# Kernel tuning notes

Measured on AMD Instinct MI355X. Metric: run time of the kernel, lower is better.

The kernel has to match this reference:

```python
import jax, jax.numpy as jnp
import numpy as np

IN_DIM = 784
HIDDEN = 512
STYLE = 128
BATCH = 2048
NUM_LABELS = 10


def setup_inputs() -> dict:
    key = jax.random.key(0)
    k1, k2, k3, k4 = jax.random.split(key, 4)
    x = jax.random.uniform(k1, (BATCH, IN_DIM), dtype=jnp.float32)
    m = jax.random.randint(k2, (BATCH,), 0, NUM_LABELS)
    # Embedding tables, scaled as in the torch __init__ (N(0,1)/fan)
    fc1_table = jax.random.normal(k3, (NUM_LABELS, (IN_DIM + 1) * HIDDEN), dtype=jnp.float32) / ((IN_DIM + 1) * HIDDEN)
    fc2_table = jax.random.normal(k4, (NUM_LABELS, (HIDDEN + 1) * STYLE), dtype=jnp.float32) / ((HIDDEN + 1) * STYLE)
    return {"x": x, "m": m, "fc1_table": fc1_table, "fc2_table": fc2_table}


def reference(x, m, fc1_table, fc2_table):
    B = x.shape[0]
    x = x.reshape(B, -1)  # [B, 784]
    # Per-sample weight matrices gathered by label
    fc1 = fc1_table[m].reshape(B, IN_DIM + 1, HIDDEN)   # [B, 785, H]
    fc1_w, fc1_b = fc1[:, :IN_DIM, :], fc1[:, -1, :]
    h1 = jax.nn.relu(jnp.einsum('bkj,bk->bj', fc1_w, x) + fc1_b)  # [B, H]
    fc2 = fc2_table[m].reshape(B, HIDDEN + 1, STYLE)    # [B, H+1, S]
    fc2_w, fc2_b = fc2[:, :HIDDEN, :], fc2[:, -1, :]
    h2 = jnp.einsum('bkj,bk->bj', fc2_w, h1) + fc2_b    # [B, S]
    return jax.nn.sigmoid(h2)
```

## Files before the change

### kernel.cpp

```cpp
#include <hip/hip_runtime.h>
#include <hip/hip_bf16.h>
#include <math.h>

#define BATCH      2048
#define IN_DIM     784
#define HIDDEN     512
#define STYLE      128
#define NUM_LABELS 10
#define FC1_STRIDE ((IN_DIM + 1) * HIDDEN)
#define FC2_STRIDE ((HIDDEN + 1) * STYLE)
#define KP1        832

#define TB        64
#define MAX_TILES 48
#define BK        64

#define META_NTILES 31
#define META_TILES  32
#define META_PERM   176

#define W1B_OFF  16384ULL
#define W2B_OFF  (W1B_OFF + 10ULL*HIDDEN*KP1*2)
#define H1B_OFF  (W2B_OFF + 10ULL*STYLE*HIDDEN*2)
#define BF16_NEED (H1B_OFF + (size_t)BATCH*HIDDEN*2)

#define W1_KB 26
#define W1_NB 16
#define W2_KB 16
#define W2_NB 4
#define W1_BLOCKS (W1_KB*W1_NB*NUM_LABELS)
#define W2_BLOCKS (W2_KB*W2_NB*NUM_LABELS)

typedef short short8  __attribute__((ext_vector_type(8)));
typedef float float4e __attribute__((ext_vector_type(4)));

__device__ __forceinline__ ushort f2b(float v) {
    __hip_bfloat16 h = __float2bfloat16(v);
    return *reinterpret_cast<ushort*>(&h);
}

__global__ void k_prep(const int* __restrict__ m, const float* __restrict__ fc1t,
                       const float* __restrict__ fc2t, int* __restrict__ meta,
                       ushort* __restrict__ w1b, ushort* __restrict__ w2b) {
    const int tid = threadIdx.x;
    int bid = blockIdx.x;

    __shared__ int cnt[NUM_LABELS], curs[NUM_LABELS], offs[NUM_LABELS + 1];
    __shared__ int permS[BATCH];
    __shared__ float tile[32][33];

    if (bid == 0) {
        if (tid < NUM_LABELS) { cnt[tid] = 0; curs[tid] = 0; }
        __syncthreads();
        for (int b = tid; b < BATCH; b += 256) atomicAdd(&cnt[m[b]], 1);
        __syncthreads();
        if (tid == 0) {
            int off = 0;
            for (int L = 0; L < NUM_LABELS; ++L) { offs[L] = off; off += cnt[L]; }
            offs[NUM_LABELS] = off;
        }
        __syncthreads();
        for (int b = tid; b < BATCH; b += 256) {
            int L = m[b];
            int r = atomicAdd(&curs[L], 1);
            permS[offs[L] + r] = b;
        }
        __syncthreads();
        for (int i = tid; i < BATCH; i += 256) meta[META_PERM + i] = permS[i];
        if (tid == 0) {
            int idx = 0;
            for (int L = 0; L < NUM_LABELS; ++L) {
                int c = cnt[L], off = offs[L];
                for (int t = 0; t < c; t += TB) {
                    meta[META_TILES + idx * 3 + 0] = L;
                    meta[META_TILES + idx * 3 + 1] = off + t;
                    meta[META_TILES + idx * 3 + 2] = min(TB, c - t);
                    ++idx;
                }
            }
            meta[META_NTILES] = idx;
        }
        return;
    }

    bid -= 1;
    const float* src; ushort* dst; int Kvalid, Kpad, N, kb, nb, L; size_t srcL, dstL;
    if (bid < W1_BLOCKS) {
        kb = bid % W1_KB; nb = (bid / W1_KB) % W1_NB; L = bid / (W1_KB * W1_NB);
        src = fc1t; dst = w1b; Kvalid = IN_DIM; Kpad = KP1; N = HIDDEN;
        srcL = FC1_STRIDE; dstL = (size_t)HIDDEN * KP1;
    } else {
        bid -= W1_BLOCKS;
        kb = bid % W2_KB; nb = (bid / W2_KB) % W2_NB; L = bid / (W2_KB * W2_NB);
        src = fc2t; dst = w2b; Kvalid = HIDDEN; Kpad = HIDDEN; N = STYLE;
        srcL = FC2_STRIDE; dstL = (size_t)STYLE * HIDDEN;
    }
    const int tx = tid & 31, ty = tid >> 5;
    const int k0 = kb * 32, n0 = nb * 32;
    for (int r = ty; r < 32; r += 8) {
        int k = k0 + r;
        tile[r][tx] = (k < Kvalid) ? src[(size_t)L * srcL + (size_t)k * N + n0 + tx] : 0.f;
    }
    __syncthreads();
    for (int r = ty; r < 32; r += 8) {
        int n = n0 + r;
        dst[(size_t)L * dstL + (size_t)n * Kpad + k0 + tx] = f2b(tile[tx][r]);
    }
}

__launch_bounds__(256)
__global__ void k_fc1m(const float* __restrict__ x, const ushort* __restrict__ w1b,
                       const float* __restrict__ fc1t, const int* __restrict__ meta,
                       ushort* __restrict__ h1b) {
    const int t = blockIdx.x;
    if (t >= meta[META_NTILES]) return;
    const int L      = meta[META_TILES + 3 * t + 0];
    const int pstart = meta[META_TILES + 3 * t + 1];
    const int nrows  = meta[META_TILES + 3 * t + 2];
    const int col0   = blockIdx.y * 64;
    const ushort* __restrict__ W = w1b + (size_t)L * HIDDEN * KP1 + (size_t)col0 * KP1;

    __shared__ int rows[TB];
    __shared__ __align__(16) ushort As[64][72];
    __shared__ __align__(16) ushort Bs[64][72];

    const int tid = threadIdx.x;
    if (tid < TB) rows[tid] = (tid < nrows) ? meta[META_PERM + pstart + tid] : -1;
    __syncthreads();

    const int sr = tid >> 2, sc = tid & 3;
    const int lane = tid & 63, wv = tid >> 6;
    const int qd = lane >> 4, ln16 = lane & 15;

    const int arow = rows[sr];
    const float* __restrict__ xr = x + (size_t)(arow < 0 ? 0 : arow) * IN_DIM;
    const uint4* __restrict__ bgp = (const uint4*)(W + (size_t)sr * KP1);

    float4e acc[4] = {};

    for (int k0 = 0; k0 < KP1; k0 += BK) {
        const int ka = k0 + sc * 16;
        float4 a0 = make_float4(0.f, 0.f, 0.f, 0.f), a1 = a0, a2 = a0, a3 = a0;
        if (arow >= 0) {
            if (ka      < IN_DIM) a0 = *(const float4*)(xr + ka);
            if (ka + 4  < IN_DIM) a1 = *(const float4*)(xr + ka + 4);
            if (ka + 8  < IN_DIM) a2 = *(const float4*)(xr + ka + 8);
            if (ka + 12 < IN_DIM) a3 = *(const float4*)(xr + ka + 12);
        }
        uint4 b0 = bgp[(k0 >> 3) + sc * 2 + 0];
        uint4 b1 = bgp[(k0 >> 3) + sc * 2 + 1];

        ushort av[16];
        av[0]=f2b(a0.x); av[1]=f2b(a0.y); av[2]=f2b(a0.z); av[3]=f2b(a0.w);
        av[4]=f2b(a1.x); av[5]=f2b(a1.y); av[6]=f2b(a1.z); av[7]=f2b(a1.w);
        av[8]=f2b(a2.x); av[9]=f2b(a2.y); av[10]=f2b(a2.z); av[11]=f2b(a2.w);
        av[12]=f2b(a3.x); av[13]=f2b(a3.y); av[14]=f2b(a3.z); av[15]=f2b(a3.w);
        *(uint4*)&As[sr][sc * 16 + 0] = *(const uint4*)&av[0];
        *(uint4*)&As[sr][sc * 16 + 8] = *(const uint4*)&av[8];
        *(uint4*)&Bs[sr][sc * 16 + 0] = b0;
        *(uint4*)&Bs[sr][sc * 16 + 8] = b1;
        __syncthreads();
#pragma unroll
        for (int s = 0; s < 2; ++s) {
            short8 a = *(const short8*)&As[wv * 16 + ln16][s * 32 + qd * 8];
#pragma unroll
            for (int nt = 0; nt < 4; ++nt) {
                short8 b = *(const short8*)&Bs[nt * 16 + ln16][s * 32 + qd * 8];
                acc[nt] = __builtin_amdgcn_mfma_f32_16x16x32_bf16(a, b, acc[nt], 0, 0, 0);
            }
        }
        __syncthreads();
    }

    const float* __restrict__ bias = fc1t + (size_t)L * FC1_STRIDE + (size_t)IN_DIM * HIDDEN + col0;
#pragma unroll
    for (int nt = 0; nt < 4; ++nt) {
        const int c = nt * 16 + ln16;
        const float bs = bias[c];
#pragma unroll
        for (int i = 0; i < 4; ++i) {
            const int r = wv * 16 + qd * 4 + i;
            if (r < nrows)
                h1b[(size_t)(pstart + r) * HIDDEN + col0 + c] = f2b(fmaxf(acc[nt][i] + bs, 0.f));
        }
    }
}

__launch_bounds__(256)
__global__ void k_fc2m(const ushort* __restrict__ h1b, const ushort* __restrict__ w2b,
                       const float* __restrict__ fc2t, const int* __restrict__ meta,
                       float* __restrict__ out) {
    const int t = blockIdx.x;
    if (t >= meta[META_NTILES]) return;
    const int L      = meta[META_TILES + 3 * t + 0];
    const int pstart = meta[META_TILES + 3 * t + 1];
    const int nrows  = meta[META_TILES + 3 * t + 2];
    const int col0   = blockIdx.y * 64;
    const ushort* __restrict__ W = w2b + (size_t)L * STYLE * HIDDEN + (size_t)col0 * HIDDEN;

    __shared__ int rows[TB];
    __shared__ __align__(16) ushort As[64][72];
    __shared__ __align__(16) ushort Bs[64][72];

    const int tid = threadIdx.x;
    if (tid < TB) rows[tid] = (tid < nrows) ? meta[META_PERM + pstart + tid] : -1;
    __syncthreads();

    const int sr = tid >> 2, sc = tid & 3;
    const int lane = tid & 63, wv = tid >> 6;
    const int qd = lane >> 4, ln16 = lane & 15;

    const bool aval = (sr < nrows);
    const uint4* __restrict__ agp = (const uint4*)(h1b + (size_t)(pstart + (aval ? sr : 0)) * HIDDEN);
    const uint4* __restrict__ bgp = (const uint4*)(W + (size_t)sr * HIDDEN);

    float4e acc[4] = {};

    for (int k0 = 0; k0 < HIDDEN; k0 += BK) {
        uint4 a0 = make_uint4(0u, 0u, 0u, 0u), a1 = a0;
        if (aval) {
            a0 = agp[(k0 >> 3) + sc * 2 + 0];
            a1 = agp[(k0 >> 3) + sc * 2 + 1];
        }
        uint4 b0 = bgp[(k0 >> 3) + sc * 2 + 0];
        uint4 b1 = bgp[(k0 >> 3) + sc * 2 + 1];
        *(uint4*)&As[sr][sc * 16 + 0] = a0;
        *(uint4*)&As[sr][sc * 16 + 8] = a1;
        *(uint4*)&Bs[sr][sc * 16 + 0] = b0;
        *(uint4*)&Bs[sr][sc * 16 + 8] = b1;
        __syncthreads();
#pragma unroll
        for (int s = 0; s < 2; ++s) {
            short8 a = *(const short8*)&As[wv * 16 + ln16][s * 32 + qd * 8];
#pragma unroll
            for (int nt = 0; nt < 4; ++nt) {
                short8 b = *(const short8*)&Bs[nt * 16 + ln16][s * 32 + qd * 8];
                acc[nt] = __builtin_amdgcn_mfma_f32_16x16x32_bf16(a, b, acc[nt], 0, 0, 0);
            }
        }
        __syncthreads();
    }

    const float* __restrict__ bias = fc2t + (size_t)L * FC2_STRIDE + (size_t)HIDDEN * STYLE + col0;
#pragma unroll
    for (int nt = 0; nt < 4; ++nt) {
        const int c = nt * 16 + ln16;
        const float bs = bias[c];
#pragma unroll
        for (int i = 0; i < 4; ++i) {
            const int r = wv * 16 + qd * 4 + i;
            if (r < nrows) {
                const int orow = rows[r];
                out[(size_t)orow * STYLE + col0 + c] = 1.f / (1.f + __expf(-(acc[nt][i] + bs)));
            }
        }
    }
}

__launch_bounds__(256)
__global__ void k_naive(const float* __restrict__ x, const int* __restrict__ m,
                        const float* __restrict__ fc1t, const float* __restrict__ fc2t,
                        float* __restrict__ out) {
    __shared__ float xs[IN_DIM];
    __shared__ float h1[HIDDEN];
    const int b = blockIdx.x, tid = threadIdx.x, L = m[b];
    for (int k = tid; k < IN_DIM; k += 256) xs[k] = x[(size_t)b * IN_DIM + k];
    __syncthreads();
    const float* __restrict__ W1 = fc1t + (size_t)L * FC1_STRIDE;
    for (int j = tid; j < HIDDEN; j += 256) {
        float acc = W1[(size_t)IN_DIM * HIDDEN + j];
        for (int k = 0; k < IN_DIM; ++k) acc = fmaf(xs[k], W1[(size_t)k * HIDDEN + j], acc);
        h1[j] = fmaxf(acc, 0.f);
    }
    __syncthreads();
    const float* __restrict__ W2 = fc2t + (size_t)L * FC2_STRIDE;
    for (int j = tid; j < STYLE; j += 256) {
        float acc = W2[(size_t)HIDDEN * STYLE + j];
        for (int k = 0; k < HIDDEN; ++k) acc = fmaf(h1[k], W2[(size_t)k * STYLE + j], acc);
        out[(size_t)b * STYLE + j] = 1.f / (1.f + __expf(-acc));
    }
}

extern "C" void kernel_launch(void* const* d_in, const int* in_sizes, int n_in,
                              void* d_out, int out_size, void* d_ws, size_t ws_size,
                              hipStream_t stream) {
    const float* x    = (const float*)d_in[0];
    const int*   m    = (const int*)d_in[1];
    const float* fc1t = (const float*)d_in[2];
    const float* fc2t = (const float*)d_in[3];
    float* out = (float*)d_out;

    if (ws_size >= BF16_NEED) {
        int*    meta = (int*)d_ws;
        ushort* w1b  = (ushort*)((char*)d_ws + W1B_OFF);
        ushort* w2b  = (ushort*)((char*)d_ws + W2B_OFF);
        ushort* h1b  = (ushort*)((char*)d_ws + H1B_OFF);

        k_prep<<<1 + W1_BLOCKS + W2_BLOCKS, 256, 0, stream>>>(m, fc1t, fc2t, meta, w1b, w2b);
        k_fc1m<<<dim3(MAX_TILES, HIDDEN / 64), 256, 0, stream>>>(x, w1b, fc1t, meta, h1b);
        k_fc2m<<<dim3(MAX_TILES, STYLE / 64), 256, 0, stream>>>(h1b, w2b, fc2t, meta, out);
    } else {
        k_naive<<<BATCH, 256, 0, stream>>>(x, m, fc1t, fc2t, out);
    }
}
```

Measured before the change: 107.0 us.

## Fuse prep, fc1 and fc2 into one persistent kernel with grid barriers

Replaces the three launches with one persistent kernel of 512 blocks that does label sorting, x and weight conversion to bf16, the fc1 GEMM and the fc2 GEMM, separated by software grid-wide barriers. x is now pre-converted to padded bf16 once, not converted inside the GEMM loop, and the GEMM loops prefetch the next K-slice into registers while the current one is computed. This removes launch gaps and repeated x conversion. In exchange it relies on all 512 blocks being co-resident for the spin barrier. It also adds the barrier cost and an extra bf16 x buffer in the workspace.

```diff
diff --git a/kernel.cpp b/kernel.cpp
--- a/kernel.cpp
+++ b/kernel.cpp
@@ -10,248 +10,269 @@
 #define FC1_STRIDE ((IN_DIM + 1) * HIDDEN)
 #define FC2_STRIDE ((HIDDEN + 1) * STYLE)
 #define KP1        832
-
-#define TB        64
-#define MAX_TILES 48
-#define BK        64
+#define TB         64
+#define BK         64
+#define NBLK       512
 
 #define META_NTILES 31
 #define META_TILES  32
 #define META_PERM   176
 
-#define W1B_OFF  16384ULL
+#define XB_OFF   16384ULL
+#define W1B_OFF  (XB_OFF  + (size_t)BATCH*KP1*2)
 #define W2B_OFF  (W1B_OFF + 10ULL*HIDDEN*KP1*2)
 #define H1B_OFF  (W2B_OFF + 10ULL*STYLE*HIDDEN*2)
-#define BF16_NEED (H1B_OFF + (size_t)BATCH*HIDDEN*2)
+#define WS_NEED  (H1B_OFF + (size_t)BATCH*HIDDEN*2)
 
 #define W1_KB 26
 #define W1_NB 16
 #define W2_KB 16
 #define W2_NB 4
-#define W1_BLOCKS (W1_KB*W1_NB*NUM_LABELS)
-#define W2_BLOCKS (W2_KB*W2_NB*NUM_LABELS)
+#define W1_TILES (W1_KB*W1_NB*NUM_LABELS)
+#define W2_TILES (W2_KB*W2_NB*NUM_LABELS)
+#define NT_TOT   (W1_TILES + W2_TILES)
+#define XCHUNKS  (BATCH * (KP1/8))
 
 typedef short short8  __attribute__((ext_vector_type(8)));
 typedef float float4e __attribute__((ext_vector_type(4)));
+
+__device__ int g_bar[2];
 
 __device__ __forceinline__ ushort f2b(float v) {
     __hip_bfloat16 h = __float2bfloat16(v);
     return *reinterpret_cast<ushort*>(&h);
 }
 
-__global__ void k_prep(const int* __restrict__ m, const float* __restrict__ fc1t,
-                       const float* __restrict__ fc2t, int* __restrict__ meta,
-                       ushort* __restrict__ w1b, ushort* __restrict__ w2b) {
-    const int tid = threadIdx.x;
-    int bid = blockIdx.x;
-
-    __shared__ int cnt[NUM_LABELS], curs[NUM_LABELS], offs[NUM_LABELS + 1];
-    __shared__ int permS[BATCH];
-    __shared__ float tile[32][33];
-
-    if (bid == 0) {
-        if (tid < NUM_LABELS) { cnt[tid] = 0; curs[tid] = 0; }
-        __syncthreads();
-        for (int b = tid; b < BATCH; b += 256) atomicAdd(&cnt[m[b]], 1);
+__device__ __forceinline__ void grid_sync(int slot) {
+    __threadfence();
+    __syncthreads();
+    if (threadIdx.x == 0) {
+        int ticket = __hip_atomic_fetch_add(&g_bar[slot], 1, __ATOMIC_ACQ_REL,
+                                            __HIP_MEMORY_SCOPE_AGENT);
+        int target = (ticket / NBLK + 1) * NBLK;
+        while (__hip_atomic_load(&g_bar[slot], __ATOMIC_ACQUIRE,
+                                 __HIP_MEMORY_SCOPE_AGENT) < target)
+            __builtin_amdgcn_s_sleep(2);
+    }
+    __syncthreads();
+    __threadfence();
+}
+
+__global__ __launch_bounds__(256, 2)
+void k_fused(const float* __restrict__ x, const int* __restrict__ m,
+             const float* __restrict__ fc1t, const float* __restrict__ fc2t,
+             char* __restrict__ ws, float* __restrict__ out) {
+    int*    meta = (int*)ws;
+    ushort* xb   = (ushort*)(ws + XB_OFF);
+    ushort* w1b  = (ushort*)(ws + W1B_OFF);
+    ushort* w2b  = (ushort*)(ws + W2B_OFF);
+    ushort* h1b  = (ushort*)(ws + H1B_OFF);
+
+    __shared__ __align__(16) char smem[64*72*2*2 + 256];
+    ushort (*As)[72] = (ushort(*)[72])smem;
+    ushort (*Bs)[72] = (ushort(*)[72])(smem + 64*72*2);
+    int*   rowsS     = (int*)(smem + 64*72*2*2);
+    float (*tileS)[36] = (float(*)[36])smem;
+    int* permS = (int*)smem;
+    int* cntS  = (int*)(smem + 8192);
+    int* cursS = (int*)(smem + 8192 + 64);
+    int* offsS = (int*)(smem + 8192 + 128);
+
+    const int tid = threadIdx.x, bid = blockIdx.x;
+
+    if (bid == NBLK - 1) {
+        if (tid < NUM_LABELS) { cntS[tid] = 0; cursS[tid] = 0; }
+        __syncthreads();
+        for (int b = tid; b < BATCH; b += 256) atomicAdd(&cntS[m[b]], 1);
         __syncthreads();
         if (tid == 0) {
             int off = 0;
-            for (int L = 0; L < NUM_LABELS; ++L) { offs[L] = off; off += cnt[L]; }
-            offs[NUM_LABELS] = off;
+            for (int L = 0; L < NUM_LABELS; ++L) { offsS[L] = off; off += cntS[L]; }
+            offsS[NUM_LABELS] = off;
         }
         __syncthreads();
         for (int b = tid; b < BATCH; b += 256) {
             int L = m[b];
-            int r = atomicAdd(&curs[L], 1);
-            permS[offs[L] + r] = b;
+            int r = atomicAdd(&cursS[L], 1);
+            permS[offsS[L] + r] = b;
         }
         __syncthreads();
         for (int i = tid; i < BATCH; i += 256) meta[META_PERM + i] = permS[i];
         if (tid == 0) {
             int idx = 0;
             for (int L = 0; L < NUM_LABELS; ++L) {
-                int c = cnt[L], off = offs[L];
+                int c = cntS[L], off = offsS[L];
                 for (int t = 0; t < c; t += TB) {
-                    meta[META_TILES + idx * 3 + 0] = L;
-                    meta[META_TILES + idx * 3 + 1] = off + t;
-                    meta[META_TILES + idx * 3 + 2] = min(TB, c - t);
+                    meta[META_TILES + idx*3 + 0] = L;
+                    meta[META_TILES + idx*3 + 1] = off + t;
+                    meta[META_TILES + idx*3 + 2] = min(TB, c - t);
                     ++idx;
                 }
             }
             meta[META_NTILES] = idx;
         }
-        return;
-    }
-
-    bid -= 1;
-    const float* src; ushort* dst; int Kvalid, Kpad, N, kb, nb, L; size_t srcL, dstL;
-    if (bid < W1_BLOCKS) {
-        kb = bid % W1_KB; nb = (bid / W1_KB) % W1_NB; L = bid / (W1_KB * W1_NB);
-        src = fc1t; dst = w1b; Kvalid = IN_DIM; Kpad = KP1; N = HIDDEN;
-        srcL = FC1_STRIDE; dstL = (size_t)HIDDEN * KP1;
     } else {
-        bid -= W1_BLOCKS;
-        kb = bid % W2_KB; nb = (bid / W2_KB) % W2_NB; L = bid / (W2_KB * W2_NB);
-        src = fc2t; dst = w2b; Kvalid = HIDDEN; Kpad = HIDDEN; N = STYLE;
-        srcL = FC2_STRIDE; dstL = (size_t)STYLE * HIDDEN;
-    }
-    const int tx = tid & 31, ty = tid >> 5;
-    const int k0 = kb * 32, n0 = nb * 32;
-    for (int r = ty; r < 32; r += 8) {
-        int k = k0 + r;
-        tile[r][tx] = (k < Kvalid) ? src[(size_t)L * srcL + (size_t)k * N + n0 + tx] : 0.f;
-    }
-    __syncthreads();
-    for (int r = ty; r < 32; r += 8) {
-        int n = n0 + r;
-        dst[(size_t)L * dstL + (size_t)n * Kpad + k0 + tx] = f2b(tile[tx][r]);
-    }
-}
-
-__launch_bounds__(256)
-__global__ void k_fc1m(const float* __restrict__ x, const ushort* __restrict__ w1b,
-                       const float* __restrict__ fc1t, const int* __restrict__ meta,
-                       ushort* __restrict__ h1b) {
-    const int t = blockIdx.x;
-    if (t >= meta[META_NTILES]) return;
-    const int L      = meta[META_TILES + 3 * t + 0];
-    const int pstart = meta[META_TILES + 3 * t + 1];
-    const int nrows  = meta[META_TILES + 3 * t + 2];
-    const int col0   = blockIdx.y * 64;
-    const ushort* __restrict__ W = w1b + (size_t)L * HIDDEN * KP1 + (size_t)col0 * KP1;
-
-    __shared__ int rows[TB];
-    __shared__ __align__(16) ushort As[64][72];
-    __shared__ __align__(16) ushort Bs[64][72];
-
-    const int tid = threadIdx.x;
-    if (tid < TB) rows[tid] = (tid < nrows) ? meta[META_PERM + pstart + tid] : -1;
-    __syncthreads();
-
+        for (int u = bid*256 + tid; u < XCHUNKS; u += (NBLK-1)*256) {
+            int row = u / 104, ka = (u - row*104) * 8;
+            uint4 o;
+            if (ka < IN_DIM) {
+                float4 p0 = *(const float4*)(x + (size_t)row*IN_DIM + ka);
+                float4 p1 = *(const float4*)(x + (size_t)row*IN_DIM + ka + 4);
+                ushort t8[8] = {f2b(p0.x), f2b(p0.y), f2b(p0.z), f2b(p0.w),
+                                f2b(p1.x), f2b(p1.y), f2b(p1.z), f2b(p1.w)};
+                o = *(const uint4*)t8;
+            } else o = make_uint4(0u, 0u, 0u, 0u);
+            *(uint4*)(xb + (size_t)row*KP1 + ka) = o;
+        }
+        for (int tt = bid; tt < NT_TOT; tt += NBLK - 1) {
+            const float* src; ushort* dst; int Kv, Kp, N, kb, nb, L; size_t sL, dL;
+            if (tt < W1_TILES) {
+                kb = tt % W1_KB; nb = (tt / W1_KB) % W1_NB; L = tt / (W1_KB * W1_NB);
+                src = fc1t; dst = w1b; Kv = IN_DIM; Kp = KP1; N = HIDDEN;
+                sL = FC1_STRIDE; dL = (size_t)HIDDEN * KP1;
+            } else {
+                int q = tt - W1_TILES;
+                kb = q % W2_KB; nb = (q / W2_KB) % W2_NB; L = q / (W2_KB * W2_NB);
+                src = fc2t; dst = w2b; Kv = HIDDEN; Kp = HIDDEN; N = STYLE;
+                sL = FC2_STRIDE; dL = (size_t)STYLE * HIDDEN;
+            }
+            const int k0 = kb*32, n0 = nb*32;
+            const int row = tid >> 3, c4 = tid & 7;
+            const int gk = k0 + row;
+            float4 v = make_float4(0.f, 0.f, 0.f, 0.f);
+            if (gk < Kv) v = *(const float4*)(src + (size_t)L*sL + (size_t)gk*N + n0 + c4*4);
+            __syncthreads();
+            *(float4*)&tileS[row][c4*4] = v;
+            __syncthreads();
+            const int on = tid >> 3, oc = tid & 7;
+            ushort4 o4;
+            o4.x = f2b(tileS[oc*4+0][on]); o4.y = f2b(tileS[oc*4+1][on]);
+            o4.z = f2b(tileS[oc*4+2][on]); o4.w = f2b(tileS[oc*4+3][on]);
+            *(ushort4*)(dst + (size_t)L*dL + (size_t)(n0+on)*Kp + k0 + oc*4) = o4;
+        }
+    }
+    grid_sync(0);
+
+    const int ntiles = meta[META_NTILES];
     const int sr = tid >> 2, sc = tid & 3;
-    const int lane = tid & 63, wv = tid >> 6;
-    const int qd = lane >> 4, ln16 = lane & 15;
-
-    const int arow = rows[sr];
-    const float* __restrict__ xr = x + (size_t)(arow < 0 ? 0 : arow) * IN_DIM;
-    const uint4* __restrict__ bgp = (const uint4*)(W + (size_t)sr * KP1);
-
-    float4e acc[4] = {};
-
-    for (int k0 = 0; k0 < KP1; k0 += BK) {
-        const int ka = k0 + sc * 16;
-        float4 a0 = make_float4(0.f, 0.f, 0.f, 0.f), a1 = a0, a2 = a0, a3 = a0;
-        if (arow >= 0) {
-            if (ka      < IN_DIM) a0 = *(const float4*)(xr + ka);
-            if (ka + 4  < IN_DIM) a1 = *(const float4*)(xr + ka + 4);
-            if (ka + 8  < IN_DIM) a2 = *(const float4*)(xr + ka + 8);
-            if (ka + 12 < IN_DIM) a3 = *(const float4*)(xr + ka + 12);
-        }
-        uint4 b0 = bgp[(k0 >> 3) + sc * 2 + 0];
-        uint4 b1 = bgp[(k0 >> 3) + sc * 2 + 1];
-
-        ushort av[16];
-        av[0]=f2b(a0.x); av[1]=f2b(a0.y); av[2]=f2b(a0.z); av[3]=f2b(a0.w);
-        av[4]=f2b(a1.x); av[5]=f2b(a1.y); av[6]=f2b(a1.z); av[7]=f2b(a1.w);
-        av[8]=f2b(a2.x); av[9]=f2b(a2.y); av[10]=f2b(a2.z); av[11]=f2b(a2.w);
-        av[12]=f2b(a3.x); av[13]=f2b(a3.y); av[14]=f2b(a3.z); av[15]=f2b(a3.w);
-        *(uint4*)&As[sr][sc * 16 + 0] = *(const uint4*)&av[0];
-        *(uint4*)&As[sr][sc * 16 + 8] = *(const uint4*)&av[8];
-        *(uint4*)&Bs[sr][sc * 16 + 0] = b0;
-        *(uint4*)&Bs[sr][sc * 16 + 8] = b1;
-        __syncthreads();
-#pragma unroll
-        for (int s = 0; s < 2; ++s) {
-            short8 a = *(const short8*)&As[wv * 16 + ln16][s * 32 + qd * 8];
-#pragma unroll
-            for (int nt = 0; nt < 4; ++nt) {
-                short8 b = *(const short8*)&Bs[nt * 16 + ln16][s * 32 + qd * 8];
-                acc[nt] = __builtin_amdgcn_mfma_f32_16x16x32_bf16(a, b, acc[nt], 0, 0, 0);
-            }
-        }
-        __syncthreads();
-    }
-
-    const float* __restrict__ bias = fc1t + (size_t)L * FC1_STRIDE + (size_t)IN_DIM * HIDDEN + col0;
-#pragma unroll
-    for (int nt = 0; nt < 4; ++nt) {
-        const int c = nt * 16 + ln16;
-        const float bs = bias[c];
-#pragma unroll
-        for (int i = 0; i < 4; ++i) {
-            const int r = wv * 16 + qd * 4 + i;
-            if (r < nrows)
-                h1b[(size_t)(pstart + r) * HIDDEN + col0 + c] = f2b(fmaxf(acc[nt][i] + bs, 0.f));
-        }
-    }
-}
-
-__launch_bounds__(256)
-__global__ void k_fc2m(const ushort* __restrict__ h1b, const ushort* __restrict__ w2b,
-                       const float* __restrict__ fc2t, const int* __restrict__ meta,
-                       float* __restrict__ out) {
-    const int t = blockIdx.x;
-    if (t >= meta[META_NTILES]) return;
-    const int L      = meta[META_TILES + 3 * t + 0];
-    const int pstart = meta[META_TILES + 3 * t + 1];
-    const int nrows  = meta[META_TILES + 3 * t + 2];
-    const int col0   = blockIdx.y * 64;
-    const ushort* __restrict__ W = w2b + (size_t)L * STYLE * HIDDEN + (size_t)col0 * HIDDEN;
-
-    __shared__ int rows[TB];
-    __shared__ __align__(16) ushort As[64][72];
-    __shared__ __align__(16) ushort Bs[64][72];
-
-    const int tid = threadIdx.x;
-    if (tid < TB) rows[tid] = (tid < nrows) ? meta[META_PERM + pstart + tid] : -1;
-    __syncthreads();
-
-    const int sr = tid >> 2, sc = tid & 3;
-    const int lane = tid & 63, wv = tid >> 6;
-    const int qd = lane >> 4, ln16 = lane & 15;
-
-    const bool aval = (sr < nrows);
-    const uint4* __restrict__ agp = (const uint4*)(h1b + (size_t)(pstart + (aval ? sr : 0)) * HIDDEN);
-    const uint4* __restrict__ bgp = (const uint4*)(W + (size_t)sr * HIDDEN);
-
-    float4e acc[4] = {};
-
-    for (int k0 = 0; k0 < HIDDEN; k0 += BK) {
-        uint4 a0 = make_uint4(0u, 0u, 0u, 0u), a1 = a0;
-        if (aval) {
-            a0 = agp[(k0 >> 3) + sc * 2 + 0];
-            a1 = agp[(k0 >> 3) + sc * 2 + 1];
-        }
-        uint4 b0 = bgp[(k0 >> 3) + sc * 2 + 0];
-        uint4 b1 = bgp[(k0 >> 3) + sc * 2 + 1];
-        *(uint4*)&As[sr][sc * 16 + 0] = a0;
-        *(uint4*)&As[sr][sc * 16 + 8] = a1;
-        *(uint4*)&Bs[sr][sc * 16 + 0] = b0;
-        *(uint4*)&Bs[sr][sc * 16 + 8] = b1;
-        __syncthreads();
-#pragma unroll
-        for (int s = 0; s < 2; ++s) {
-            short8 a = *(const short8*)&As[wv * 16 + ln16][s * 32 + qd * 8];
-#pragma unroll
-            for (int nt = 0; nt < 4; ++nt) {
-                short8 b = *(const short8*)&Bs[nt * 16 + ln16][s * 32 + qd * 8];
-                acc[nt] = __builtin_amdgcn_mfma_f32_16x16x32_bf16(a, b, acc[nt], 0, 0, 0);
-            }
-        }
-        __syncthreads();
-    }
-
-    const float* __restrict__ bias = fc2t + (size_t)L * FC2_STRIDE + (size_t)HIDDEN * STYLE + col0;
-#pragma unroll
-    for (int nt = 0; nt < 4; ++nt) {
-        const int c = nt * 16 + ln16;
-        const float bs = bias[c];
-#pragma unroll
-        for (int i = 0; i < 4; ++i) {
-            const int r = wv * 16 + qd * 4 + i;
-            if (r < nrows) {
-                const int orow = rows[r];
-                out[(size_t)orow * STYLE + col0 + c] = 1.f / (1.f + __expf(-(acc[nt][i] + bs)));
+    const int lane = tid & 63, wv = tid >> 6, qd = lane >> 4, ln16 = lane & 15;
+
+    for (int j = bid; j < ntiles * 8; j += NBLK) {
+        const int t = j >> 3, cb = j & 7;
+        const int L      = meta[META_TILES + 3*t + 0];
+        const int pstart = meta[META_TILES + 3*t + 1];
+        const int nrows  = meta[META_TILES + 3*t + 2];
+        const int col0   = cb * 64;
+        __syncthreads();
+        if (tid < TB) rowsS[tid] = (tid < nrows) ? meta[META_PERM + pstart + tid] : -1;
+        __syncthreads();
+        const int arow = rowsS[sr];
+        const bool aval = (arow >= 0);
+        const uint4* __restrict__ agp = (const uint4*)(xb + (size_t)(aval ? arow : 0) * KP1);
+        const uint4* __restrict__ bgp = (const uint4*)(w1b + (size_t)L*HIDDEN*KP1 + (size_t)(col0 + sr)*KP1);
+
+        float4e acc[4] = {};
+        uint4 a0, a1, b0, b1;
+        {
+            const int base = sc * 2;
+            a0 = aval ? agp[base] : make_uint4(0u,0u,0u,0u);
+            a1 = aval ? agp[base+1] : make_uint4(0u,0u,0u,0u);
+            b0 = bgp[base]; b1 = bgp[base+1];
+        }
+        for (int it = 0; it < KP1/BK; ++it) {
+            *(uint4*)&As[sr][sc*16 + 0] = a0;
+            *(uint4*)&As[sr][sc*16 + 8] = a1;
+            *(uint4*)&Bs[sr][sc*16 + 0] = b0;
+            *(uint4*)&Bs[sr][sc*16 + 8] = b1;
+            __syncthreads();
+            if (it + 1 < KP1/BK) {
+                const int base = (it+1)*8 + sc*2;
+                a0 = aval ? agp[base] : make_uint4(0u,0u,0u,0u);
+                a1 = aval ? agp[base+1] : make_uint4(0u,0u,0u,0u);
+                b0 = bgp[base]; b1 = bgp[base+1];
+            }
+#pragma unroll
+            for (int s = 0; s < 2; ++s) {
+                short8 af = *(const short8*)&As[wv*16 + ln16][s*32 + qd*8];
+#pragma unroll
+                for (int nt = 0; nt < 4; ++nt) {
+                    short8 bf = *(const short8*)&Bs[nt*16 + ln16][s*32 + qd*8];
+                    acc[nt] = __builtin_amdgcn_mfma_f32_16x16x32_bf16(af, bf, acc[nt], 0, 0, 0);
+                }
+            }
+            __syncthreads();
+        }
+        const float* __restrict__ bias = fc1t + (size_t)L*FC1_STRIDE + (size_t)IN_DIM*HIDDEN + col0;
+#pragma unroll
+        for (int nt = 0; nt < 4; ++nt) {
+            const int c = nt*16 + ln16;
+            const float bs = bias[c];
+#pragma unroll
+            for (int i = 0; i < 4; ++i) {
+                const int r = wv*16 + qd*4 + i;
+                if (r < nrows)
+                    h1b[(size_t)(pstart + r)*HIDDEN + col0 + c] = f2b(fmaxf(acc[nt][i] + bs, 0.f));
+            }
+        }
+    }
+    grid_sync(1);
+
+    for (int j = bid; j < ntiles * 2; j += NBLK) {
+        const int t = j >> 1, cb = j & 1;
+        const int L      = meta[META_TILES + 3*t + 0];
+        const int pstart = meta[META_TILES + 3*t + 1];
+        const int nrows  = meta[META_TILES + 3*t + 2];
+        const int col0   = cb * 64;
+        __syncthreads();
+        if (tid < TB) rowsS[tid] = (tid < nrows) ? meta[META_PERM + pstart + tid] : -1;
+        __syncthreads();
+        const bool aval = (sr < nrows);
+        const uint4* __restrict__ agp = (const uint4*)(h1b + (size_t)(pstart + (aval ? sr : 0))*HIDDEN);
+        const uint4* __restrict__ bgp = (const uint4*)(w2b + (size_t)L*STYLE*HIDDEN + (size_t)(col0 + sr)*HIDDEN);
+
+        float4e acc[4] = {};
+        uint4 a0, a1, b0, b1;
+        {
+            const int base = sc * 2;
+            a0 = aval ? agp[base] : make_uint4(0u,0u,0u,0u);
+            a1 = aval ? agp[base+1] : make_uint4(0u,0u,0u,0u);
+            b0 = bgp[base]; b1 = bgp[base+1];
+        }
+        for (int it = 0; it < HIDDEN/BK; ++it) {
+            *(uint4*)&As[sr][sc*16 + 0] = a0;
+            *(uint4*)&As[sr][sc*16 + 8] = a1;
+            *(uint4*)&Bs[sr][sc*16 + 0] = b0;
+            *(uint4*)&Bs[sr][sc*16 + 8] = b1;
+            __syncthreads();
+            if (it + 1 < HIDDEN/BK) {
+                const int base = (it+1)*8 + sc*2;
+                a0 = aval ? agp[base] : make_uint4(0u,0u,0u,0u);
+                a1 = aval ? agp[base+1] : make_uint4(0u,0u,0u,0u);
+                b0 = bgp[base]; b1 = bgp[base+1];
+            }
+#pragma unroll
+            for (int s = 0; s < 2; ++s) {
+                short8 af = *(const short8*)&As[wv*16 + ln16][s*32 + qd*8];
+#pragma unroll
+                for (int nt = 0; nt < 4; ++nt) {
+                    short8 bf = *(const short8*)&Bs[nt*16 + ln16][s*32 + qd*8];
+                    acc[nt] = __builtin_amdgcn_mfma_f32_16x16x32_bf16(af, bf, acc[nt], 0, 0, 0);
+                }
+            }
+            __syncthreads();
+        }
+        const float* __restrict__ bias = fc2t + (size_t)L*FC2_STRIDE + (size_t)HIDDEN*STYLE + col0;
+#pragma unroll
+        for (int nt = 0; nt < 4; ++nt) {
+            const int c = nt*16 + ln16;
+            const float bs = bias[c];
+#pragma unroll
+            for (int i = 0; i < 4; ++i) {
+                const int r = wv*16 + qd*4 + i;
+                if (r < nrows) {
+                    const int orow = rowsS[r];
+                    out[(size_t)orow*STYLE + col0 + c] = 1.f / (1.f + __expf(-(acc[nt][i] + bs)));
+                }
             }
         }
     }
@@ -264,20 +285,20 @@
     __shared__ float xs[IN_DIM];
     __shared__ float h1[HIDDEN];
     const int b = blockIdx.x, tid = threadIdx.x, L = m[b];
-    for (int k = tid; k < IN_DIM; k += 256) xs[k] = x[(size_t)b * IN_DIM + k];
+    for (int k = tid; k < IN_DIM; k += 256) xs[k] = x[(size_t)b*IN_DIM + k];
     __syncthreads();
-    const float* __restrict__ W1 = fc1t + (size_t)L * FC1_STRIDE;
+    const float* __restrict__ W1 = fc1t + (size_t)L*FC1_STRIDE;
     for (int j = tid; j < HIDDEN; j += 256) {
-        float acc = W1[(size_t)IN_DIM * HIDDEN + j];
-        for (int k = 0; k < IN_DIM; ++k) acc = fmaf(xs[k], W1[(size_t)k * HIDDEN + j], acc);
+        float acc = W1[(size_t)IN_DIM*HIDDEN + j];
+        for (int k = 0; k < IN_DIM; ++k) acc = fmaf(xs[k], W1[(size_t)k*HIDDEN + j], acc);
         h1[j] = fmaxf(acc, 0.f);
     }
     __syncthreads();
-    const float* __restrict__ W2 = fc2t + (size_t)L * FC2_STRIDE;
+    const float* __restrict__ W2 = fc2t + (size_t)L*FC2_STRIDE;
     for (int j = tid; j < STYLE; j += 256) {
-        float acc = W2[(size_t)HIDDEN * STYLE + j];
-        for (int k = 0; k < HIDDEN; ++k) acc = fmaf(h1[k], W2[(size_t)k * STYLE + j], acc);
-        out[(size_t)b * STYLE + j] = 1.f / (1.f + __expf(-acc));
+        float acc = W2[(size_t)HIDDEN*STYLE + j];
+        for (int k = 0; k < HIDDEN; ++k) acc = fmaf(h1[k], W2[(size_t)k*STYLE + j], acc);
+        out[(size_t)b*STYLE + j] = 1.f / (1.f + __expf(-acc));
     }
 }
 
@@ -290,15 +311,8 @@
     const float* fc2t = (const float*)d_in[3];
     float* out = (float*)d_out;
 
-    if (ws_size >= BF16_NEED) {
-        int*    meta = (int*)d_ws;
-        ushort* w1b  = (ushort*)((char*)d_ws + W1B_OFF);
-        ushort* w2b  = (ushort*)((char*)d_ws + W2B_OFF);
-        ushort* h1b  = (ushort*)((char*)d_ws + H1B_OFF);
-
-        k_prep<<<1 + W1_BLOCKS + W2_BLOCKS, 256, 0, stream>>>(m, fc1t, fc2t, meta, w1b, w2b);
-        k_fc1m<<<dim3(MAX_TILES, HIDDEN / 64), 256, 0, stream>>>(x, w1b, fc1t, meta, h1b);
-        k_fc2m<<<dim3(MAX_TILES, STYLE / 64), 256, 0, stream>>>(h1b, w2b, fc2t, meta, out);
+    if (ws_size >= WS_NEED) {
+        k_fused<<<NBLK, 256, 0, stream>>>(x, m, fc1t, fc2t, (char*)d_ws, out);
     } else {
         k_naive<<<BATCH, 256, 0, stream>>>(x, m, fc1t, fc2t, out);
     }
```

Result: slower. 370.0 us (+245.9%).

## Fuse fc1 and fc2 into one kernel with the hidden tile kept in LDS

Applied to the files above, without the earlier changes.

Replaces the separate fc1 and fc2 grouped-GEMM kernels with a single k_mlp kernel. Each block takes a 32-row tile of one label and computes all 512 hidden columns, writes ReLU(h1) as bf16 into shared memory, then runs fc2 from LDS. The aim is to remove the h1 round-trip through global memory and one kernel launch. Weight and activation tiles are prefetched into registers for the next k-step. The trade-off is far fewer blocks (about 80 instead of 384), a large LDS footprint per block, and every block re-reading the full per-label W1 from cache.

```diff
diff --git a/kernel.cpp b/kernel.cpp
--- a/kernel.cpp
+++ b/kernel.cpp
@@ -10,19 +10,16 @@
 #define FC1_STRIDE ((IN_DIM + 1) * HIDDEN)
 #define FC2_STRIDE ((HIDDEN + 1) * STYLE)
 #define KP1        832
-
-#define TB        64
-#define MAX_TILES 48
-#define BK        64
+#define TB2        32
+#define MAXT2      80
 
 #define META_NTILES 31
 #define META_TILES  32
-#define META_PERM   176
+#define META_PERM   288
 
 #define W1B_OFF  16384ULL
 #define W2B_OFF  (W1B_OFF + 10ULL*HIDDEN*KP1*2)
-#define H1B_OFF  (W2B_OFF + 10ULL*STYLE*HIDDEN*2)
-#define BF16_NEED (H1B_OFF + (size_t)BATCH*HIDDEN*2)
+#define WS_NEED  (W2B_OFF + 10ULL*STYLE*HIDDEN*2)
 
 #define W1_KB 26
 #define W1_NB 16
@@ -31,6 +28,11 @@
 #define W1_BLOCKS (W1_KB*W1_NB*NUM_LABELS)
 #define W2_BLOCKS (W2_KB*W2_NB*NUM_LABELS)
 
+#define SM_AS_OFF   128
+#define SM_BS_OFF   (SM_AS_OFF + 32*72*2)
+#define SM_H1_OFF   (SM_BS_OFF + 512*72*2)
+#define SM_BYTES    (SM_H1_OFF + 32*520*2)
+
 typedef short short8  __attribute__((ext_vector_type(8)));
 typedef float float4e __attribute__((ext_vector_type(4)));
 
@@ -71,10 +73,10 @@
             int idx = 0;
             for (int L = 0; L < NUM_LABELS; ++L) {
                 int c = cnt[L], off = offs[L];
-                for (int t = 0; t < c; t += TB) {
+                for (int t = 0; t < c; t += TB2) {
                     meta[META_TILES + idx * 3 + 0] = L;
                     meta[META_TILES + idx * 3 + 1] = off + t;
-                    meta[META_TILES + idx * 3 + 2] = min(TB, c - t);
+                    meta[META_TILES + idx * 3 + 2] = min(TB2, c - t);
                     ++idx;
                 }
             }
@@ -108,151 +110,163 @@
     }
 }
 
-__launch_bounds__(256)
-__global__ void k_fc1m(const float* __restrict__ x, const ushort* __restrict__ w1b,
-                       const float* __restrict__ fc1t, const int* __restrict__ meta,
-                       ushort* __restrict__ h1b) {
+__global__ __launch_bounds__(256, 1)
+void k_mlp(const float* __restrict__ x, const float* __restrict__ fc1t,
+           const float* __restrict__ fc2t, const ushort* __restrict__ w1b,
+           const ushort* __restrict__ w2b, const int* __restrict__ meta,
+           float* __restrict__ out) {
     const int t = blockIdx.x;
     if (t >= meta[META_NTILES]) return;
-    const int L      = meta[META_TILES + 3 * t + 0];
-    const int pstart = meta[META_TILES + 3 * t + 1];
-    const int nrows  = meta[META_TILES + 3 * t + 2];
-    const int col0   = blockIdx.y * 64;
-    const ushort* __restrict__ W = w1b + (size_t)L * HIDDEN * KP1 + (size_t)col0 * KP1;
-
-    __shared__ int rows[TB];
-    __shared__ __align__(16) ushort As[64][72];
-    __shared__ __align__(16) ushort Bs[64][72];
+    const int L      = meta[META_TILES + 3*t + 0];
+    const int pstart = meta[META_TILES + 3*t + 1];
+    const int nrows  = meta[META_TILES + 3*t + 2];
+
+    extern __shared__ __align__(16) char smem[];
+    int*    rowsS       = (int*)smem;
+    ushort (*As)[72]    = (ushort(*)[72])(smem + SM_AS_OFF);
+    ushort (*Bs)[72]    = (ushort(*)[72])(smem + SM_BS_OFF);
+    ushort (*h1S)[520]  = (ushort(*)[520])(smem + SM_H1_OFF);
 
     const int tid = threadIdx.x;
-    if (tid < TB) rows[tid] = (tid < nrows) ? meta[META_PERM + pstart + tid] : -1;
-    __syncthreads();
-
-    const int sr = tid >> 2, sc = tid & 3;
-    const int lane = tid & 63, wv = tid >> 6;
-    const int qd = lane >> 4, ln16 = lane & 15;
-
-    const int arow = rows[sr];
+    if (tid < TB2) rowsS[tid] = (tid < nrows) ? meta[META_PERM + pstart + tid] : -1;
+    __syncthreads();
+
+    const int lane = tid & 63, wv = tid >> 6, qd = lane >> 4, ln16 = lane & 15;
+
+    const int ar = tid >> 3, akc = tid & 7;
+    const int arow = rowsS[ar];
     const float* __restrict__ xr = x + (size_t)(arow < 0 ? 0 : arow) * IN_DIM;
-    const uint4* __restrict__ bgp = (const uint4*)(W + (size_t)sr * KP1);
-
-    float4e acc[4] = {};
-
-    for (int k0 = 0; k0 < KP1; k0 += BK) {
-        const int ka = k0 + sc * 16;
-        float4 a0 = make_float4(0.f, 0.f, 0.f, 0.f), a1 = a0, a2 = a0, a3 = a0;
-        if (arow >= 0) {
-            if (ka      < IN_DIM) a0 = *(const float4*)(xr + ka);
-            if (ka + 4  < IN_DIM) a1 = *(const float4*)(xr + ka + 4);
-            if (ka + 8  < IN_DIM) a2 = *(const float4*)(xr + ka + 8);
-            if (ka + 12 < IN_DIM) a3 = *(const float4*)(xr + ka + 12);
-        }
-        uint4 b0 = bgp[(k0 >> 3) + sc * 2 + 0];
-        uint4 b1 = bgp[(k0 >> 3) + sc * 2 + 1];
-
-        ushort av[16];
-        av[0]=f2b(a0.x); av[1]=f2b(a0.y); av[2]=f2b(a0.z); av[3]=f2b(a0.w);
-        av[4]=f2b(a1.x); av[5]=f2b(a1.y); av[6]=f2b(a1.z); av[7]=f2b(a1.w);
-        av[8]=f2b(a2.x); av[9]=f2b(a2.y); av[10]=f2b(a2.z); av[11]=f2b(a2.w);
-        av[12]=f2b(a3.x); av[13]=f2b(a3.y); av[14]=f2b(a3.z); av[15]=f2b(a3.w);
-        *(uint4*)&As[sr][sc * 16 + 0] = *(const uint4*)&av[0];
-        *(uint4*)&As[sr][sc * 16 + 8] = *(const uint4*)&av[8];
-        *(uint4*)&Bs[sr][sc * 16 + 0] = b0;
-        *(uint4*)&Bs[sr][sc * 16 + 8] = b1;
-        __syncthreads();
+    const ushort* __restrict__ wbase = w1b + (size_t)L * HIDDEN * KP1;
+
+    float4e acc[2][8] = {};
+    float4 a0 = make_float4(0.f,0.f,0.f,0.f), a1 = a0;
+    uint4 bpf[16];
+    {
+        const int ka = akc * 8;
+        if (arow >= 0 && ka < IN_DIM) {
+            a0 = *(const float4*)(xr + ka);
+            a1 = *(const float4*)(xr + ka + 4);
+        }
+#pragma unroll
+        for (int r = 0; r < 16; ++r) {
+            const int idx = r*256 + tid, n = idx >> 3, c = idx & 7;
+            bpf[r] = *(const uint4*)(wbase + (size_t)n * KP1 + c*8);
+        }
+    }
+
+    for (int it = 0; it < KP1/64; ++it) {
+        {
+            ushort av[8] = {f2b(a0.x), f2b(a0.y), f2b(a0.z), f2b(a0.w),
+                            f2b(a1.x), f2b(a1.y), f2b(a1.z), f2b(a1.w)};
+            *(uint4*)&As[ar][akc*8] = *(const uint4*)av;
+        }
+#pragma unroll
+        for (int r = 0; r < 16; ++r) {
+            const int idx = r*256 + tid, n = idx >> 3, c = idx & 7;
+            *(uint4*)&Bs[n][c*8] = bpf[r];
+        }
+        __syncthreads();
+
+        if (it + 1 < KP1/64) {
+            const int k0 = (it+1)*64, ka = k0 + akc*8;
+            a0 = make_float4(0.f,0.f,0.f,0.f); a1 = a0;
+            if (arow >= 0 && ka < IN_DIM) {
+                a0 = *(const float4*)(xr + ka);
+                a1 = *(const float4*)(xr + ka + 4);
+            }
+#pragma unroll
+            for (int r = 0; r < 16; ++r) {
+                const int idx = r*256 + tid, n = idx >> 3, c = idx & 7;
+                bpf[r] = *(const uint4*)(wbase + (size_t)n * KP1 + k0 + c*8);
+            }
+        }
+
 #pragma unroll
         for (int s = 0; s < 2; ++s) {
-            short8 a = *(const short8*)&As[wv * 16 + ln16][s * 32 + qd * 8];
-#pragma unroll
-            for (int nt = 0; nt < 4; ++nt) {
-                short8 b = *(const short8*)&Bs[nt * 16 + ln16][s * 32 + qd * 8];
-                acc[nt] = __builtin_amdgcn_mfma_f32_16x16x32_bf16(a, b, acc[nt], 0, 0, 0);
-            }
-        }
-        __syncthreads();
-    }
-
-    const float* __restrict__ bias = fc1t + (size_t)L * FC1_STRIDE + (size_t)IN_DIM * HIDDEN + col0;
-#pragma unroll
-    for (int nt = 0; nt < 4; ++nt) {
-        const int c = nt * 16 + ln16;
-        const float bs = bias[c];
-#pragma unroll
-        for (int i = 0; i < 4; ++i) {
-            const int r = wv * 16 + qd * 4 + i;
-            if (r < nrows)
-                h1b[(size_t)(pstart + r) * HIDDEN + col0 + c] = f2b(fmaxf(acc[nt][i] + bs, 0.f));
-        }
-    }
-}
-
-__launch_bounds__(256)
-__global__ void k_fc2m(const ushort* __restrict__ h1b, const ushort* __restrict__ w2b,
-                       const float* __restrict__ fc2t, const int* __restrict__ meta,
-                       float* __restrict__ out) {
-    const int t = blockIdx.x;
-    if (t >= meta[META_NTILES]) return;
-    const int L      = meta[META_TILES + 3 * t + 0];
-    const int pstart = meta[META_TILES + 3 * t + 1];
-    const int nrows  = meta[META_TILES + 3 * t + 2];
-    const int col0   = blockIdx.y * 64;
-    const ushort* __restrict__ W = w2b + (size_t)L * STYLE * HIDDEN + (size_t)col0 * HIDDEN;
-
-    __shared__ int rows[TB];
-    __shared__ __align__(16) ushort As[64][72];
-    __shared__ __align__(16) ushort Bs[64][72];
-
-    const int tid = threadIdx.x;
-    if (tid < TB) rows[tid] = (tid < nrows) ? meta[META_PERM + pstart + tid] : -1;
-    __syncthreads();
-
-    const int sr = tid >> 2, sc = tid & 3;
-    const int lane = tid & 63, wv = tid >> 6;
-    const int qd = lane >> 4, ln16 = lane & 15;
-
-    const bool aval = (sr < nrows);
-    const uint4* __restrict__ agp = (const uint4*)(h1b + (size_t)(pstart + (aval ? sr : 0)) * HIDDEN);
-    const uint4* __restrict__ bgp = (const uint4*)(W + (size_t)sr * HIDDEN);
-
-    float4e acc[4] = {};
-
-    for (int k0 = 0; k0 < HIDDEN; k0 += BK) {
-        uint4 a0 = make_uint4(0u, 0u, 0u, 0u), a1 = a0;
-        if (aval) {
-            a0 = agp[(k0 >> 3) + sc * 2 + 0];
-            a1 = agp[(k0 >> 3) + sc * 2 + 1];
-        }
-        uint4 b0 = bgp[(k0 >> 3) + sc * 2 + 0];
-        uint4 b1 = bgp[(k0 >> 3) + sc * 2 + 1];
-        *(uint4*)&As[sr][sc * 16 + 0] = a0;
-        *(uint4*)&As[sr][sc * 16 + 8] = a1;
-        *(uint4*)&Bs[sr][sc * 16 + 0] = b0;
-        *(uint4*)&Bs[sr][sc * 16 + 8] = b1;
-        __syncthreads();
-#pragma unroll
-        for (int s = 0; s < 2; ++s) {
-            short8 a = *(const short8*)&As[wv * 16 + ln16][s * 32 + qd * 8];
-#pragma unroll
-            for (int nt = 0; nt < 4; ++nt) {
-                short8 b = *(const short8*)&Bs[nt * 16 + ln16][s * 32 + qd * 8];
-                acc[nt] = __builtin_amdgcn_mfma_f32_16x16x32_bf16(a, b, acc[nt], 0, 0, 0);
-            }
-        }
-        __syncthreads();
-    }
-
-    const float* __restrict__ bias = fc2t + (size_t)L * FC2_STRIDE + (size_t)HIDDEN * STYLE + col0;
-#pragma unroll
-    for (int nt = 0; nt < 4; ++nt) {
-        const int c = nt * 16 + ln16;
-        const float bs = bias[c];
-#pragma unroll
-        for (int i = 0; i < 4; ++i) {
-            const int r = wv * 16 + qd * 4 + i;
-            if (r < nrows) {
-                const int orow = rows[r];
-                out[(size_t)orow * STYLE + col0 + c] = 1.f / (1.f + __expf(-(acc[nt][i] + bs)));
-            }
+            short8 af0 = *(const short8*)&As[ln16][s*32 + qd*8];
+            short8 af1 = *(const short8*)&As[16 + ln16][s*32 + qd*8];
+#pragma unroll
+            for (int cf = 0; cf < 8; ++cf) {
+                short8 bf = *(const short8*)&Bs[wv*128 + cf*16 + ln16][s*32 + qd*8];
+                acc[0][cf] = __builtin_amdgcn_mfma_f32_16x16x32_bf16(af0, bf, acc[0][cf], 0,0,0);
+                acc[1][cf] = __builtin_amdgcn_mfma_f32_16x16x32_bf16(af1, bf, acc[1][cf], 0,0,0);
+            }
+        }
+        __syncthreads();
+    }
+
+    {
+        const float* __restrict__ b1p = fc1t + (size_t)L*FC1_STRIDE + (size_t)IN_DIM*HIDDEN;
+#pragma unroll
+        for (int cf = 0; cf < 8; ++cf) {
+            const int col = wv*128 + cf*16 + ln16;
+            const float bs = b1p[col];
+#pragma unroll
+            for (int rf = 0; rf < 2; ++rf)
+#pragma unroll
+                for (int i = 0; i < 4; ++i) {
+                    const int row = rf*16 + qd*4 + i;
+                    h1S[row][col] = f2b(fmaxf(acc[rf][cf][i] + bs, 0.f));
+                }
+        }
+    }
+    __syncthreads();
+
+    const ushort* __restrict__ w2base = w2b + (size_t)L * STYLE * HIDDEN;
+    ushort (*Bs2)[136] = (ushort(*)[136])&Bs[0][0];
+
+    float4e acc2[2][2] = {};
+    uint4 b2pf[8];
+#pragma unroll
+    for (int r = 0; r < 8; ++r) {
+        const int idx = r*256 + tid, n = idx >> 4, c = idx & 15;
+        b2pf[r] = *(const uint4*)(w2base + (size_t)n * HIDDEN + c*8);
+    }
+    for (int it = 0; it < 4; ++it) {
+#pragma unroll
+        for (int r = 0; r < 8; ++r) {
+            const int idx = r*256 + tid, n = idx >> 4, c = idx & 15;
+            *(uint4*)&Bs2[n][c*8] = b2pf[r];
+        }
+        __syncthreads();
+        if (it + 1 < 4) {
+            const int k0 = (it+1)*128;
+#pragma unroll
+            for (int r = 0; r < 8; ++r) {
+                const int idx = r*256 + tid, n = idx >> 4, c = idx & 15;
+                b2pf[r] = *(const uint4*)(w2base + (size_t)n * HIDDEN + k0 + c*8);
+            }
+        }
+#pragma unroll
+        for (int s = 0; s < 4; ++s) {
+            short8 af0 = *(const short8*)&h1S[ln16][it*128 + s*32 + qd*8];
+            short8 af1 = *(const short8*)&h1S[16 + ln16][it*128 + s*32 + qd*8];
+#pragma unroll
+            for (int cf = 0; cf < 2; ++cf) {
+                short8 bf = *(const short8*)&Bs2[wv*32 + cf*16 + ln16][s*32 + qd*8];
+                acc2[0][cf] = __builtin_amdgcn_mfma_f32_16x16x32_bf16(af0, bf, acc2[0][cf], 0,0,0);
+                acc2[1][cf] = __builtin_amdgcn_mfma_f32_16x16x32_bf16(af1, bf, acc2[1][cf], 0,0,0);
+            }
+        }
+        __syncthreads();
+    }
+
+    {
+        const float* __restrict__ b2p = fc2t + (size_t)L*FC2_STRIDE + (size_t)HIDDEN*STYLE;
+#pragma unroll
+        for (int cf = 0; cf < 2; ++cf) {
+            const int col = wv*32 + cf*16 + ln16;
+            const float bs = b2p[col];
+#pragma unroll
+            for (int rf = 0; rf < 2; ++rf)
+#pragma unroll
+                for (int i = 0; i < 4; ++i) {
+                    const int row = rf*16 + qd*4 + i;
+                    if (row < nrows) {
+                        const int orow = rowsS[row];
+                        out[(size_t)orow*STYLE + col] = 1.f / (1.f + __expf(-(acc2[rf][cf][i] + bs)));
+                    }
+                }
         }
     }
 }
@@ -290,15 +304,13 @@
     const float* fc2t = (const float*)d_in[3];
     float* out = (float*)d_out;
 
-    if (ws_size >= BF16_NEED) {
+    if (ws_size >= WS_NEED) {
         int*    meta = (int*)d_ws;
         ushort* w1b  = (ushort*)((char*)d_ws + W1B_OFF);
         ushort* w2b  = (ushort*)((char*)d_ws + W2B_OFF);
-        ushort* h1b  = (ushort*)((char*)d_ws + H1B_OFF);
 
         k_prep<<<1 + W1_BLOCKS + W2_BLOCKS, 256, 0, stream>>>(m, fc1t, fc2t, meta, w1b, w2b);
-        k_fc1m<<<dim3(MAX_TILES, HIDDEN / 64), 256, 0, stream>>>(x, w1b, fc1t, meta, h1b);
-        k_fc2m<<<dim3(MAX_TILES, STYLE / 64), 256, 0, stream>>>(h1b, w2b, fc2t, meta, out);
+        k_mlp<<<MAXT2, 256, SM_BYTES, stream>>>(x, fc1t, fc2t, w1b, w2b, meta, out);
     } else {
         k_naive<<<BATCH, 256, 0, stream>>>(x, m, fc1t, fc2t, out);
     }
```

Result: slower. 206.1 us (+92.7%).
